# Performance work log

Measured on AMD Instinct MI355X. Metric: run time of the kernel, lower is better.

Reference implementation:

```python
import jax, jax.numpy as jnp
import numpy as np

U = 100000  # num_users
I = 100000  # num_items
D = 64      # dims
L = 50      # seq_L


def setup_inputs() -> dict:
    key = jax.random.key(0)
    ks = jax.random.split(key, 12)
    B, T = 4096, 100
    inp = {
        "user_ids": jax.random.randint(ks[0], (B,), 0, U),
        "item_seq_ids": jax.random.randint(ks[1], (B, L), 0, I),
        "target_item_ids": jax.random.randint(ks[2], (B, T), 0, I),
        # embedding tables (normal init)
        "user_table": jax.random.normal(ks[3], (U, D), jnp.float32) * 0.01,
        "item_table": jax.random.normal(ks[4], (I, D), jnp.float32) * 0.01,
        "W2_table": jax.random.normal(ks[5], (I, D), jnp.float32) * 0.01,
        "b2_table": jnp.zeros((I, 1), jnp.float32),
        # feature gates: Linear(dims, dims), he_uniform weight, zero bias
        "fg_item_W": jax.random.uniform(ks[6], (D, D), jnp.float32, -1.0, 1.0) * np.sqrt(6.0 / D),
        "fg_item_b": jnp.zeros((D,), jnp.float32),
        "fg_user_W": jax.random.uniform(ks[7], (D, D), jnp.float32, -1.0, 1.0) * np.sqrt(6.0 / D),
        "fg_user_b": jnp.zeros((D,), jnp.float32),
        # instance gates: xavier_uniform
        "inst_gate_item": jax.random.uniform(ks[8], (D, 1), jnp.float32, -1.0, 1.0) * np.sqrt(6.0 / (D + 1)),
        "inst_gate_user": jax.random.uniform(ks[9], (D, L), jnp.float32, -1.0, 1.0) * np.sqrt(6.0 / (D + L)),
    }
    return inp


def _forward_user(user_emb, item_embs, fg_item_W, fg_item_b, fg_user_W, fg_user_b,
                  inst_gate_item, inst_gate_user):
    # user_emb: [B,D], item_embs: [B,L,D]
    gate = jax.nn.sigmoid(
        item_embs @ fg_item_W.T + fg_item_b
        + (user_emb @ fg_user_W.T + fg_user_b)[:, None, :]
    )  # [B,L,D]
    gated = item_embs * gate  # [B,L,D]
    term1 = jnp.einsum("bld,d->bl", gated, inst_gate_item[:, 0])
    term2 = user_emb @ inst_gate_user  # [B,L]
    inst = jax.nn.sigmoid(term1 + term2)  # [B,L]
    union = jnp.sum(gated * inst[:, :, None], axis=1)  # [B,D]
    union = union / jnp.sum(inst, axis=1, keepdims=True)
    return union


def reference(user_ids, item_seq_ids, target_item_ids, user_table, item_table,
              W2_table, b2_table, fg_item_W, fg_item_b, fg_user_W, fg_user_b,
              inst_gate_item, inst_gate_user):
    item_embs = item_table[item_seq_ids]      # [B,L,D]
    user_emb = user_table[user_ids]           # [B,D]
    union = _forward_user(user_emb, item_embs, fg_item_W, fg_item_b,
                          fg_user_W, fg_user_b, inst_gate_item, inst_gate_user)
    w2 = W2_table[target_item_ids]            # [B,T,D]
    b2 = b2_table[target_item_ids][..., 0]    # [B,T]
    res = b2 + jnp.einsum("btd,bd->bt", w2, user_emb)
    res = res + jnp.einsum("bd,btd->bt", union, w2)
    # rel_score: bmm(item_embs, w2^T) summed over L == contract item_embs summed over L with w2
    res = res + jnp.einsum("bd,btd->bt", jnp.sum(item_embs, axis=1), w2)
    return res
```

## Files before the change

### kernel.cpp

```cpp
#include <hip/hip_runtime.h>

#define DD 64
#define LL 50
#define NB 4096
#define NT 100

typedef __attribute__((ext_vector_type(8))) __bf16 bf16x8;
typedef __attribute__((ext_vector_type(4))) float f32x4;

__device__ __forceinline__ float sigmoidf_(float x) {
    return __builtin_amdgcn_rcpf(1.0f + __expf(-x));
}
__device__ __forceinline__ unsigned pack_bf16(float hi, float lo) {
    union { float f; unsigned u; } a, b;
    a.f = hi; b.f = lo;
    return ((a.u + 0x8000u) & 0xffff0000u) | ((b.u + 0x8000u) >> 16);
}
__device__ __forceinline__ uint4 cvt8u(const float* f) {
    uint4 r;
    r.x = pack_bf16(f[1], f[0]);
    r.y = pack_bf16(f[3], f[2]);
    r.z = pack_bf16(f[5], f[4]);
    r.w = pack_bf16(f[7], f[6]);
    return r;
}
__device__ __forceinline__ bf16x8 cvt8(const float* f) {
    return __builtin_bit_cast(bf16x8, cvt8u(f));
}
__device__ __forceinline__ unsigned cvtpk(float lo, float hi) {
    unsigned r;
    asm("v_cvt_pk_bf16_f32 %0, %1, %2" : "=v"(r) : "v"(lo), "v"(hi));
    return r;
}
__device__ __forceinline__ bf16x8 cvt8f(const float* f) {
    uint4 r;
    r.x = cvtpk(f[0], f[1]);
    r.y = cvtpk(f[2], f[3]);
    r.z = cvtpk(f[4], f[5]);
    r.w = cvtpk(f[6], f[7]);
    return __builtin_bit_cast(bf16x8, r);
}
__device__ __forceinline__ void glds16(const float* g, float* l) {
    __builtin_amdgcn_global_load_lds(
        (const __attribute__((address_space(1))) void*)g,
        (__attribute__((address_space(3))) void*)l, 16, 0, 0);
}
__device__ __forceinline__ void glds4(const float* g, float* l) {
    __builtin_amdgcn_global_load_lds(
        (const __attribute__((address_space(1))) void*)g,
        (__attribute__((address_space(3))) void*)l, 4, 0, 0);
}

__global__ __launch_bounds__(128) void k0_user(
    const int* __restrict__ uid_g, const float* __restrict__ user_table,
    const float* __restrict__ Wu, const float* __restrict__ bu,
    const float* __restrict__ bi, const float* __restrict__ igu,
    const float* __restrict__ Wi,
    float* __restrict__ ufg_ws, float* __restrict__ t2_ws,
    unsigned short* __restrict__ wiB_ws)
{
    if (blockIdx.x == 256) {
        if (threadIdx.x >= 64) return;
        const int n = threadIdx.x;
        float tmp[64];
#pragma unroll
        for (int c4 = 0; c4 < 16; c4++)
            *(float4*)&tmp[c4 * 4] = *(const float4*)(Wi + n * DD + c4 * 4);
#pragma unroll
        for (int ch = 0; ch < 8; ch++)
            *(uint4*)(wiB_ws + n * DD + ch * 8) = cvt8u(tmp + ch * 8);
        return;
    }

    const int lane = threadIdx.x & 63;
    const int wv = threadIdx.x >> 6;
    const int c = lane & 15, q = lane >> 4;
    const int uid = uid_g[blockIdx.x * 16 + c];
    const float* urow = user_table + (size_t)uid * DD;

    bf16x8 af[2];
#pragma unroll
    for (int kf = 0; kf < 2; kf++) {
        float tmp[8];
        *(float4*)&tmp[0] = *(const float4*)(urow + kf * 32 + q * 8);
        *(float4*)&tmp[4] = *(const float4*)(urow + kf * 32 + q * 8 + 4);
        af[kf] = cvt8(tmp);
    }

#pragma unroll
    for (int ni0 = 0; ni0 < 4; ni0++) {
        const int ni = wv * 4 + ni0;
        f32x4 a = {0.f, 0.f, 0.f, 0.f};
#pragma unroll
        for (int kf = 0; kf < 2; kf++) {
            const int k0 = kf * 32 + q * 8;
            float tmp[8];
            if (ni < 4) {
                const float* src = Wu + (ni * 16 + c) * DD + k0;
                *(float4*)&tmp[0] = *(const float4*)src;
                *(float4*)&tmp[4] = *(const float4*)(src + 4);
            } else {
                const int l = ni * 16 + c - 64;
#pragma unroll
                for (int j = 0; j < 8; j++)
                    tmp[j] = (l < LL) ? igu[(k0 + j) * LL + l] : 0.f;
            }
            a = __builtin_amdgcn_mfma_f32_16x16x32_bf16(af[kf], cvt8(tmp), a, 0, 0, 0);
        }
        const int n = ni * 16 + c;
#pragma unroll
        for (int reg = 0; reg < 4; reg++) {
            const int bo = blockIdx.x * 16 + q * 4 + reg;
            if (n < DD)           ufg_ws[bo * DD + n] = a[reg] + bu[n] + bi[n];
            else if (n < DD + LL) t2_ws[bo * DD + (n - DD)] = a[reg];
        }
    }
}

__global__ __launch_bounds__(256, 4) void k1_fused(
    const int* __restrict__ uid_g, const int* __restrict__ iid_g,
    const int* __restrict__ tgt_g,
    const float* __restrict__ user_table, const float* __restrict__ item_table,
    const float* __restrict__ W2, const float* __restrict__ b2,
    const unsigned short* __restrict__ wiB, const float* __restrict__ igi,
    const float* __restrict__ ufg_ws, const float* __restrict__ t2_ws,
    float* __restrict__ out)
{
    const int tid = threadIdx.x;
    const int lane = tid & 63;
    const int w = tid >> 6;
    const int c = lane & 15, q = lane >> 4;
    const int j = tid & 15, gg = tid >> 4;
    const int b = blockIdx.x;

    __shared__ __align__(16) float sE[4][16 * DD];
    __shared__ __align__(16) float sB[128];
    __shared__ __align__(16) float sUu[DD];
    __shared__ __align__(16) float sU[4 * DD];
    __shared__ __align__(16) float sS[4 * DD];
    __shared__ float sI[4];
    __shared__ float sOut[112];

    const int* iidp = iid_g + b * LL;
    const int* tgtp = tgt_g + b * NT;
    float* sEw = sE[w];

    int iid4[4];
#pragma unroll
    for (int s = 0; s < 4; s++) {
        const int r = w * 16 + 4 * s + (lane >> 4);
        iid4[s] = iidp[r < LL ? r : LL - 1];
    }
    int tt[7];
#pragma unroll
    for (int i = 0; i < 7; i++) {
        const int ts = i * 16 + gg;
        tt[i] = tgtp[ts < NT ? ts : NT - 1];
    }

#pragma unroll
    for (int s = 0; s < 4; s++) {
        const int rl = 4 * s + (lane >> 4);
        const int j2 = (lane & 15) ^ (rl & 7);
        glds16(item_table + (size_t)iid4[s] * DD + j2 * 4, sEw + s * 256);
    }

    float4 wv[7];
#pragma unroll
    for (int i = 0; i < 7; i++)
        wv[i] = *(const float4*)(W2 + (size_t)tt[i] * DD + j * 4);

    if (w == 1) {
        const int uid = uid_g[b];
        glds4(user_table + (size_t)uid * DD + lane, sUu);
    }
    if (w == 2) {
        const int tb = lane < NT ? lane : NT - 1;
        glds4(b2 + tgtp[tb], sB);
    }
    if (w == 3) {
        const int sl = 64 + lane;
        const int tb = sl < NT ? sl : NT - 1;
        glds4(b2 + tgtp[tb], sB + 64);
    }

    float ufg4[4], igi4[4];
#pragma unroll
    for (int ni = 0; ni < 4; ni++) {
        ufg4[ni] = ufg_ws[b * DD + ni * 16 + c];
        igi4[ni] = igi[ni * 16 + c];
    }
    const float4 t2v = *(const float4*)(t2_ws + b * DD + w * 16 + q * 4);
    float t2a[4] = {t2v.x, t2v.y, t2v.z, t2v.w};

    bf16x8 wb[4][2];
#pragma unroll
    for (int ni = 0; ni < 4; ni++)
#pragma unroll
        for (int kf = 0; kf < 2; kf++)
            wb[ni][kf] = __builtin_bit_cast(bf16x8,
                *(const uint4*)(wiB + (ni * 16 + c) * DD + kf * 32 + q * 8));

    asm volatile("s_waitcnt vmcnt(0)" ::: "memory");
    __builtin_amdgcn_sched_barrier(0);

    bf16x8 ea[2];
    {
        const int grow = w * 16 + c;
        const float* rowp = sEw + c * DD;
        const int s7 = c & 7;
#pragma unroll
        for (int kf = 0; kf < 2; kf++) {
            float tmp[8];
            const int ch0 = (kf * 8 + 2 * q) ^ s7;
            const int ch1 = (kf * 8 + 2 * q + 1) ^ s7;
            *(float4*)&tmp[0] = *(const float4*)(rowp + ch0 * 4);
            *(float4*)&tmp[4] = *(const float4*)(rowp + ch1 * 4);
            if (grow >= LL) {
#pragma unroll
                for (int i = 0; i < 8; i++) tmp[i] = 0.f;
            }
            ea[kf] = cvt8f(tmp);
        }
    }

    float unum[4] = {0.f, 0.f, 0.f, 0.f};
    float sip[4]  = {0.f, 0.f, 0.f, 0.f};
    float isum = 0.f;
    {
        f32x4 acc[4];
#pragma unroll
        for (int ni = 0; ni < 4; ni++) {
            f32x4 a = {0.f, 0.f, 0.f, 0.f};
            a = __builtin_amdgcn_mfma_f32_16x16x32_bf16(ea[0], wb[ni][0], a, 0, 0, 0);
            a = __builtin_amdgcn_mfma_f32_16x16x32_bf16(ea[1], wb[ni][1], a, 0, 0, 0);
            acc[ni] = a;
        }
#pragma unroll
        for (int reg = 0; reg < 4; reg++) {
            const int lrl = q * 4 + reg;
            const int valid = (w * 16 + lrl < LL);
            const int s7 = lrl & 7;
            float gd[4];
            float t1 = 0.f;
#pragma unroll
            for (int ni = 0; ni < 4; ni++) {
                const int phys = (4 * ni + (c >> 2)) ^ s7;
                const float ev = sEw[lrl * DD + phys * 4 + (c & 3)];
                const float e = valid ? ev : 0.f;
                const float g = sigmoidf_(acc[ni][reg] + ufg4[ni]);
                gd[ni] = e * g;
                t1 += gd[ni] * igi4[ni];
                sip[ni] += e;
            }
            t1 += __shfl_xor(t1, 1); t1 += __shfl_xor(t1, 2);
            t1 += __shfl_xor(t1, 4); t1 += __shfl_xor(t1, 8);
            const float inst = valid ? sigmoidf_(t1 + t2a[reg]) : 0.f;
            isum += inst;
#pragma unroll
            for (int ni = 0; ni < 4; ni++)
                unum[ni] += gd[ni] * inst;
        }
    }

#pragma unroll
    for (int ni = 0; ni < 4; ni++) {
        unum[ni] += __shfl_xor(unum[ni], 16); unum[ni] += __shfl_xor(unum[ni], 32);
        sip[ni]  += __shfl_xor(sip[ni], 16);  sip[ni]  += __shfl_xor(sip[ni], 32);
    }
    isum += __shfl_xor(isum, 16); isum += __shfl_xor(isum, 32);

    const float un = (q == 0) ? unum[0] : (q == 1) ? unum[1] : (q == 2) ? unum[2] : unum[3];
    const float si = (q == 0) ? sip[0]  : (q == 1) ? sip[1]  : (q == 2) ? sip[2]  : sip[3];
    sU[w * DD + lane] = un;
    sS[w * DD + lane] = si;
    if (lane == 0) sI[w] = isum;
    __syncthreads();

    float4 vr;
    {
        const float4 u0 = *(const float4*)&sU[0 * DD + j * 4];
        const float4 u1 = *(const float4*)&sU[1 * DD + j * 4];
        const float4 u2 = *(const float4*)&sU[2 * DD + j * 4];
        const float4 u3 = *(const float4*)&sU[3 * DD + j * 4];
        const float4 s0 = *(const float4*)&sS[0 * DD + j * 4];
        const float4 s1 = *(const float4*)&sS[1 * DD + j * 4];
        const float4 s2 = *(const float4*)&sS[2 * DD + j * 4];
        const float4 s3 = *(const float4*)&sS[3 * DD + j * 4];
        const float4 uu = *(const float4*)&sUu[j * 4];
        const float rist = __builtin_amdgcn_rcpf(sI[0] + sI[1] + sI[2] + sI[3]);
        vr.x = uu.x + (u0.x + u1.x + u2.x + u3.x) * rist + (s0.x + s1.x + s2.x + s3.x);
        vr.y = uu.y + (u0.y + u1.y + u2.y + u3.y) * rist + (s0.y + s1.y + s2.y + s3.y);
        vr.z = uu.z + (u0.z + u1.z + u2.z + u3.z) * rist + (s0.z + s1.z + s2.z + s3.z);
        vr.w = uu.w + (u0.w + u1.w + u2.w + u3.w) * rist + (s0.w + s1.w + s2.w + s3.w);
    }

#pragma unroll
    for (int i = 0; i < 7; i++) {
        const int ts = i * 16 + gg;
        float s = wv[i].x * vr.x + wv[i].y * vr.y + wv[i].z * vr.z + wv[i].w * vr.w;
        s += __shfl_xor(s, 1); s += __shfl_xor(s, 2);
        s += __shfl_xor(s, 4); s += __shfl_xor(s, 8);
        if (j == 0 && ts < NT) sOut[ts] = s + sB[ts];
    }
    __syncthreads();
    if (tid < NT) out[b * NT + tid] = sOut[tid];
}

extern "C" void kernel_launch(void* const* d_in, const int* in_sizes, int n_in,
                              void* d_out, int out_size, void* d_ws, size_t ws_size,
                              hipStream_t stream)
{
    const int* user_ids        = (const int*)d_in[0];
    const int* item_seq_ids    = (const int*)d_in[1];
    const int* target_item_ids = (const int*)d_in[2];
    const float* user_tab      = (const float*)d_in[3];
    const float* item_tab      = (const float*)d_in[4];
    const float* W2_tab        = (const float*)d_in[5];
    const float* b2_tab        = (const float*)d_in[6];
    const float* fg_item_W     = (const float*)d_in[7];
    const float* fg_item_b     = (const float*)d_in[8];
    const float* fg_user_W     = (const float*)d_in[9];
    const float* fg_user_b     = (const float*)d_in[10];
    const float* igi           = (const float*)d_in[11];
    const float* igu           = (const float*)d_in[12];
    float* out = (float*)d_out;

    float* ufg_ws = (float*)d_ws;
    float* t2_ws  = ufg_ws + NB * DD;
    unsigned short* wiB_ws = (unsigned short*)(t2_ws + NB * DD);

    k0_user<<<257, 128, 0, stream>>>(user_ids, user_tab, fg_user_W, fg_user_b,
                                     fg_item_b, igu, fg_item_W,
                                     ufg_ws, t2_ws, wiB_ws);
    k1_fused<<<NB, 256, 0, stream>>>(user_ids, item_seq_ids, target_item_ids,
                                     user_tab, item_tab, W2_tab, b2_tab,
                                     wiB_ws, igi, ufg_ws, t2_ws, out);
}
```

Baseline: 153.6 us.

## Process four batch rows per block with double-buffered gather prefetch

k1_fused now handles NITER=4 batch rows per block, loading each next row's item embeddings, W2 rows, user row and biases into a second LDS/register buffer while the current row is computed. The fc_item weight copy and workspace values are pre-scaled by -log2(e), so each sigmoid uses exp2 directly instead of exp. The ufg workspace is stored in a permuted layout so each lane reads it with one float4 load. This trades a 4x smaller grid, doubled LDS and more registers (the occupancy hint of 4 blocks is dropped) for hiding gather latency and amortising the per-block weight loads.

```diff
diff --git a/kernel.cpp b/kernel.cpp
--- a/kernel.cpp
+++ b/kernel.cpp
@@ -4,12 +4,14 @@
 #define LL 50
 #define NB 4096
 #define NT 100
+#define NITER 4
+#define NEGK (-1.44269504088896f)
 
 typedef __attribute__((ext_vector_type(8))) __bf16 bf16x8;
 typedef __attribute__((ext_vector_type(4))) float f32x4;
 
-__device__ __forceinline__ float sigmoidf_(float x) {
-    return __builtin_amdgcn_rcpf(1.0f + __expf(-x));
+__device__ __forceinline__ float sig2_(float y) {
+    return __builtin_amdgcn_rcpf(1.0f + __builtin_amdgcn_exp2f(y));
 }
 __device__ __forceinline__ unsigned pack_bf16(float hi, float lo) {
     union { float f; unsigned u; } a, b;
@@ -67,6 +69,8 @@
         for (int c4 = 0; c4 < 16; c4++)
             *(float4*)&tmp[c4 * 4] = *(const float4*)(Wi + n * DD + c4 * 4);
 #pragma unroll
+        for (int kk = 0; kk < 64; kk++) tmp[kk] *= NEGK;
+#pragma unroll
         for (int ch = 0; ch < 8; ch++)
             *(uint4*)(wiB_ws + n * DD + ch * 8) = cvt8u(tmp + ch * 8);
         return;
@@ -102,8 +106,8 @@
             } else {
                 const int l = ni * 16 + c - 64;
 #pragma unroll
-                for (int j = 0; j < 8; j++)
-                    tmp[j] = (l < LL) ? igu[(k0 + j) * LL + l] : 0.f;
+                for (int jj = 0; jj < 8; jj++)
+                    tmp[jj] = (l < LL) ? igu[(k0 + jj) * LL + l] : 0.f;
             }
             a = __builtin_amdgcn_mfma_f32_16x16x32_bf16(af[kf], cvt8(tmp), a, 0, 0, 0);
         }
@@ -111,13 +115,15 @@
 #pragma unroll
         for (int reg = 0; reg < 4; reg++) {
             const int bo = blockIdx.x * 16 + q * 4 + reg;
-            if (n < DD)           ufg_ws[bo * DD + n] = a[reg] + bu[n] + bi[n];
-            else if (n < DD + LL) t2_ws[bo * DD + (n - DD)] = a[reg];
+            if (n < DD)
+                ufg_ws[bo * DD + (n & 15) * 4 + (n >> 4)] = NEGK * (a[reg] + bu[n] + bi[n]);
+            else if (n < DD + LL)
+                t2_ws[bo * DD + (n - DD)] = NEGK * a[reg];
         }
     }
 }
 
-__global__ __launch_bounds__(256, 4) void k1_fused(
+__global__ __launch_bounds__(256) void k1_fused(
     const int* __restrict__ uid_g, const int* __restrict__ iid_g,
     const int* __restrict__ tgt_g,
     const float* __restrict__ user_table, const float* __restrict__ item_table,
@@ -131,68 +137,19 @@
     const int w = tid >> 6;
     const int c = lane & 15, q = lane >> 4;
     const int j = tid & 15, gg = tid >> 4;
-    const int b = blockIdx.x;
-
-    __shared__ __align__(16) float sE[4][16 * DD];
-    __shared__ __align__(16) float sB[128];
-    __shared__ __align__(16) float sUu[DD];
+    const int b0 = blockIdx.x * NITER;
+
+    __shared__ __align__(16) float sE[2][4][16 * DD];
+    __shared__ __align__(16) float sUu[2][DD];
+    __shared__ __align__(16) float sB[2][128];
     __shared__ __align__(16) float sU[4 * DD];
     __shared__ __align__(16) float sS[4 * DD];
     __shared__ float sI[4];
     __shared__ float sOut[112];
 
-    const int* iidp = iid_g + b * LL;
-    const int* tgtp = tgt_g + b * NT;
-    float* sEw = sE[w];
-
-    int iid4[4];
-#pragma unroll
-    for (int s = 0; s < 4; s++) {
-        const int r = w * 16 + 4 * s + (lane >> 4);
-        iid4[s] = iidp[r < LL ? r : LL - 1];
-    }
-    int tt[7];
-#pragma unroll
-    for (int i = 0; i < 7; i++) {
-        const int ts = i * 16 + gg;
-        tt[i] = tgtp[ts < NT ? ts : NT - 1];
-    }
-
-#pragma unroll
-    for (int s = 0; s < 4; s++) {
-        const int rl = 4 * s + (lane >> 4);
-        const int j2 = (lane & 15) ^ (rl & 7);
-        glds16(item_table + (size_t)iid4[s] * DD + j2 * 4, sEw + s * 256);
-    }
-
-    float4 wv[7];
-#pragma unroll
-    for (int i = 0; i < 7; i++)
-        wv[i] = *(const float4*)(W2 + (size_t)tt[i] * DD + j * 4);
-
-    if (w == 1) {
-        const int uid = uid_g[b];
-        glds4(user_table + (size_t)uid * DD + lane, sUu);
-    }
-    if (w == 2) {
-        const int tb = lane < NT ? lane : NT - 1;
-        glds4(b2 + tgtp[tb], sB);
-    }
-    if (w == 3) {
-        const int sl = 64 + lane;
-        const int tb = sl < NT ? sl : NT - 1;
-        glds4(b2 + tgtp[tb], sB + 64);
-    }
-
-    float ufg4[4], igi4[4];
-#pragma unroll
-    for (int ni = 0; ni < 4; ni++) {
-        ufg4[ni] = ufg_ws[b * DD + ni * 16 + c];
-        igi4[ni] = igi[ni * 16 + c];
-    }
-    const float4 t2v = *(const float4*)(t2_ws + b * DD + w * 16 + q * 4);
-    float t2a[4] = {t2v.x, t2v.y, t2v.z, t2v.w};
-
+    float igi4[4];
+#pragma unroll
+    for (int ni = 0; ni < 4; ni++) igi4[ni] = igi[ni * 16 + c] * NEGK;
     bf16x8 wb[4][2];
 #pragma unroll
     for (int ni = 0; ni < 4; ni++)
@@ -201,110 +158,174 @@
             wb[ni][kf] = __builtin_bit_cast(bf16x8,
                 *(const uint4*)(wiB + (ni * 16 + c) * DD + kf * 32 + q * 8));
 
+    int iidA[4], ttA[7], uidA = 0, tqA = 0;
+    int iidB[4], ttB[7], uidB = 0, tqB = 0;
+    float4 wvb[2][7];
+    float4 ufgv[2], t2v[2];
+
+#define LOADQ(bb, iid_, tt_, uid_, tq_) do {                                   \
+        const int* iidp_ = iid_g + (bb) * LL;                                  \
+        const int* tgtp_ = tgt_g + (bb) * NT;                                  \
+        _Pragma("unroll") for (int s = 0; s < 4; s++) {                        \
+            const int r_ = w * 16 + 4 * s + q;                                 \
+            iid_[s] = iidp_[r_ < LL ? r_ : LL - 1]; }                          \
+        _Pragma("unroll") for (int i = 0; i < 7; i++) {                        \
+            const int ts_ = i * 16 + gg;                                       \
+            tt_[i] = tgtp_[ts_ < NT ? ts_ : NT - 1]; }                         \
+        uid_ = uid_g[bb];                                                      \
+        if (w == 2) tq_ = tgtp_[lane < NT ? lane : NT - 1];                    \
+        if (w == 3) { const int sl_ = 64 + lane;                               \
+                      tq_ = tgtp_[sl_ < NT ? sl_ : NT - 1]; }                  \
+    } while (0)
+
+#define ISSUEP(bb, p_, iid_, tt_, uid_, tq_) do {                              \
+        float* sEw_ = sE[p_][w];                                               \
+        _Pragma("unroll") for (int s = 0; s < 4; s++) {                        \
+            const int rl_ = 4 * s + q;                                         \
+            const int j2_ = c ^ (rl_ & 7);                                     \
+            glds16(item_table + (size_t)iid_[s] * DD + j2_ * 4,                \
+                   sEw_ + s * 256); }                                          \
+        _Pragma("unroll") for (int i = 0; i < 7; i++)                          \
+            wvb[p_][i] = *(const float4*)(W2 + (size_t)tt_[i] * DD + j * 4);   \
+        ufgv[p_] = *(const float4*)(ufg_ws + (size_t)(bb) * DD + c * 4);       \
+        t2v[p_]  = *(const float4*)(t2_ws + (size_t)(bb) * DD + w * 16 + q * 4);\
+        if (w == 1) glds4(user_table + (size_t)uid_ * DD + lane, sUu[p_]);     \
+        if (w == 2) glds4(b2 + tq_, sB[p_]);                                   \
+        if (w == 3) glds4(b2 + tq_, sB[p_] + 64);                              \
+    } while (0)
+
+    LOADQ(b0, iidA, ttA, uidA, tqA);
     asm volatile("s_waitcnt vmcnt(0)" ::: "memory");
     __builtin_amdgcn_sched_barrier(0);
-
-    bf16x8 ea[2];
-    {
-        const int grow = w * 16 + c;
-        const float* rowp = sEw + c * DD;
-        const int s7 = c & 7;
-#pragma unroll
-        for (int kf = 0; kf < 2; kf++) {
-            float tmp[8];
-            const int ch0 = (kf * 8 + 2 * q) ^ s7;
-            const int ch1 = (kf * 8 + 2 * q + 1) ^ s7;
-            *(float4*)&tmp[0] = *(const float4*)(rowp + ch0 * 4);
-            *(float4*)&tmp[4] = *(const float4*)(rowp + ch1 * 4);
-            if (grow >= LL) {
-#pragma unroll
-                for (int i = 0; i < 8; i++) tmp[i] = 0.f;
+    ISSUEP(b0, 0, iidA, ttA, uidA, tqA);
+    LOADQ(b0 + 1, iidB, ttB, uidB, tqB);
+
+#pragma unroll
+    for (int it = 0; it < NITER; ++it) {
+        const int p = it & 1;
+        const int bb = b0 + it;
+
+        asm volatile("s_waitcnt vmcnt(0)" ::: "memory");
+        __builtin_amdgcn_sched_barrier(0);
+
+        if (it + 1 < NITER) {
+            if ((it & 1) == 0) ISSUEP(bb + 1, 1, iidB, ttB, uidB, tqB);
+            else               ISSUEP(bb + 1, 0, iidA, ttA, uidA, tqA);
+        }
+        if (it + 2 < NITER) {
+            if ((it & 1) == 0) LOADQ(bb + 2, iidA, ttA, uidA, tqA);
+            else               LOADQ(bb + 2, iidB, ttB, uidB, tqB);
+        }
+
+        const float* sEw = sE[p][w];
+        const float ufg_n[4] = {ufgv[p].x, ufgv[p].y, ufgv[p].z, ufgv[p].w};
+        const float t2a[4]   = {t2v[p].x, t2v[p].y, t2v[p].z, t2v[p].w};
+
+        bf16x8 ea[2];
+        {
+            const int grow = w * 16 + c;
+            const float* rowp = sEw + c * DD;
+            const int s7 = c & 7;
+#pragma unroll
+            for (int kf = 0; kf < 2; kf++) {
+                float tmp[8];
+                const int ch0 = (kf * 8 + 2 * q) ^ s7;
+                const int ch1 = (kf * 8 + 2 * q + 1) ^ s7;
+                *(float4*)&tmp[0] = *(const float4*)(rowp + ch0 * 4);
+                *(float4*)&tmp[4] = *(const float4*)(rowp + ch1 * 4);
+                if (grow >= LL) {
+#pragma unroll
+                    for (int i = 0; i < 8; i++) tmp[i] = 0.f;
+                }
+                ea[kf] = cvt8f(tmp);
             }
-            ea[kf] = cvt8f(tmp);
-        }
+        }
+
+        float unum[4] = {0.f, 0.f, 0.f, 0.f};
+        float sip[4]  = {0.f, 0.f, 0.f, 0.f};
+        float isum = 0.f;
+        {
+            f32x4 acc[4];
+#pragma unroll
+            for (int ni = 0; ni < 4; ni++) {
+                f32x4 a = {0.f, 0.f, 0.f, 0.f};
+                a = __builtin_amdgcn_mfma_f32_16x16x32_bf16(ea[0], wb[ni][0], a, 0, 0, 0);
+                a = __builtin_amdgcn_mfma_f32_16x16x32_bf16(ea[1], wb[ni][1], a, 0, 0, 0);
+                acc[ni] = a;
+            }
+#pragma unroll
+            for (int reg = 0; reg < 4; reg++) {
+                const int lrl = q * 4 + reg;
+                const int valid = (w * 16 + lrl < LL);
+                const int s7 = lrl & 7;
+                float gd[4];
+                float t1 = 0.f;
+#pragma unroll
+                for (int ni = 0; ni < 4; ni++) {
+                    const int phys = (4 * ni + (c >> 2)) ^ s7;
+                    const float ev = sEw[lrl * DD + phys * 4 + (c & 3)];
+                    const float e = valid ? ev : 0.f;
+                    const float g = sig2_(acc[ni][reg] + ufg_n[ni]);
+                    gd[ni] = e * g;
+                    t1 += gd[ni] * igi4[ni];
+                    sip[ni] += e;
+                }
+                t1 += __shfl_xor(t1, 1); t1 += __shfl_xor(t1, 2);
+                t1 += __shfl_xor(t1, 4); t1 += __shfl_xor(t1, 8);
+                const float inst = valid ? sig2_(t1 + t2a[reg]) : 0.f;
+                isum += inst;
+#pragma unroll
+                for (int ni = 0; ni < 4; ni++)
+                    unum[ni] += gd[ni] * inst;
+            }
+        }
+
+#pragma unroll
+        for (int ni = 0; ni < 4; ni++) {
+            unum[ni] += __shfl_xor(unum[ni], 16); unum[ni] += __shfl_xor(unum[ni], 32);
+            sip[ni]  += __shfl_xor(sip[ni], 16);  sip[ni]  += __shfl_xor(sip[ni], 32);
+        }
+        isum += __shfl_xor(isum, 16); isum += __shfl_xor(isum, 32);
+
+        const float un = (q == 0) ? unum[0] : (q == 1) ? unum[1] : (q == 2) ? unum[2] : unum[3];
+        const float si = (q == 0) ? sip[0]  : (q == 1) ? sip[1]  : (q == 2) ? sip[2]  : sip[3];
+        sU[w * DD + lane] = un;
+        sS[w * DD + lane] = si;
+        if (lane == 0) sI[w] = isum;
+        __syncthreads();
+
+        float4 vr;
+        {
+            const float4 u0 = *(const float4*)&sU[0 * DD + j * 4];
+            const float4 u1 = *(const float4*)&sU[1 * DD + j * 4];
+            const float4 u2 = *(const float4*)&sU[2 * DD + j * 4];
+            const float4 u3 = *(const float4*)&sU[3 * DD + j * 4];
+            const float4 s0 = *(const float4*)&sS[0 * DD + j * 4];
+            const float4 s1 = *(const float4*)&sS[1 * DD + j * 4];
+            const float4 s2 = *(const float4*)&sS[2 * DD + j * 4];
+            const float4 s3 = *(const float4*)&sS[3 * DD + j * 4];
+            const float4 uu = *(const float4*)&sUu[p][j * 4];
+            const float rist = __builtin_amdgcn_rcpf(sI[0] + sI[1] + sI[2] + sI[3]);
+            vr.x = uu.x + (u0.x + u1.x + u2.x + u3.x) * rist + (s0.x + s1.x + s2.x + s3.x);
+            vr.y = uu.y + (u0.y + u1.y + u2.y + u3.y) * rist + (s0.y + s1.y + s2.y + s3.y);
+            vr.z = uu.z + (u0.z + u1.z + u2.z + u3.z) * rist + (s0.z + s1.z + s2.z + s3.z);
+            vr.w = uu.w + (u0.w + u1.w + u2.w + u3.w) * rist + (s0.w + s1.w + s2.w + s3.w);
+        }
+
+#pragma unroll
+        for (int i = 0; i < 7; i++) {
+            const int ts = i * 16 + gg;
+            float s = wvb[p][i].x * vr.x + wvb[p][i].y * vr.y
+                    + wvb[p][i].z * vr.z + wvb[p][i].w * vr.w;
+            s += __shfl_xor(s, 1); s += __shfl_xor(s, 2);
+            s += __shfl_xor(s, 4); s += __shfl_xor(s, 8);
+            if (j == 0 && ts < NT) sOut[ts] = s + sB[p][ts];
+        }
+        __syncthreads();
+        if (tid < NT) out[bb * NT + tid] = sOut[tid];
     }
-
-    float unum[4] = {0.f, 0.f, 0.f, 0.f};
-    float sip[4]  = {0.f, 0.f, 0.f, 0.f};
-    float isum = 0.f;
-    {
-        f32x4 acc[4];
-#pragma unroll
-        for (int ni = 0; ni < 4; ni++) {
-            f32x4 a = {0.f, 0.f, 0.f, 0.f};
-            a = __builtin_amdgcn_mfma_f32_16x16x32_bf16(ea[0], wb[ni][0], a, 0, 0, 0);
-            a = __builtin_amdgcn_mfma_f32_16x16x32_bf16(ea[1], wb[ni][1], a, 0, 0, 0);
-            acc[ni] = a;
-        }
-#pragma unroll
-        for (int reg = 0; reg < 4; reg++) {
-            const int lrl = q * 4 + reg;
-            const int valid = (w * 16 + lrl < LL);
-            const int s7 = lrl & 7;
-            float gd[4];
-            float t1 = 0.f;
-#pragma unroll
-            for (int ni = 0; ni < 4; ni++) {
-                const int phys = (4 * ni + (c >> 2)) ^ s7;
-                const float ev = sEw[lrl * DD + phys * 4 + (c & 3)];
-                const float e = valid ? ev : 0.f;
-                const float g = sigmoidf_(acc[ni][reg] + ufg4[ni]);
-                gd[ni] = e * g;
-                t1 += gd[ni] * igi4[ni];
-                sip[ni] += e;
-            }
-            t1 += __shfl_xor(t1, 1); t1 += __shfl_xor(t1, 2);
-            t1 += __shfl_xor(t1, 4); t1 += __shfl_xor(t1, 8);
-            const float inst = valid ? sigmoidf_(t1 + t2a[reg]) : 0.f;
-            isum += inst;
-#pragma unroll
-            for (int ni = 0; ni < 4; ni++)
-                unum[ni] += gd[ni] * inst;
-        }
-    }
-
-#pragma unroll
-    for (int ni = 0; ni < 4; ni++) {
-        unum[ni] += __shfl_xor(unum[ni], 16); unum[ni] += __shfl_xor(unum[ni], 32);
-        sip[ni]  += __shfl_xor(sip[ni], 16);  sip[ni]  += __shfl_xor(sip[ni], 32);
-    }
-    isum += __shfl_xor(isum, 16); isum += __shfl_xor(isum, 32);
-
-    const float un = (q == 0) ? unum[0] : (q == 1) ? unum[1] : (q == 2) ? unum[2] : unum[3];
-    const float si = (q == 0) ? sip[0]  : (q == 1) ? sip[1]  : (q == 2) ? sip[2]  : sip[3];
-    sU[w * DD + lane] = un;
-    sS[w * DD + lane] = si;
-    if (lane == 0) sI[w] = isum;
-    __syncthreads();
-
-    float4 vr;
-    {
-        const float4 u0 = *(const float4*)&sU[0 * DD + j * 4];
-        const float4 u1 = *(const float4*)&sU[1 * DD + j * 4];
-        const float4 u2 = *(const float4*)&sU[2 * DD + j * 4];
-        const float4 u3 = *(const float4*)&sU[3 * DD + j * 4];
-        const float4 s0 = *(const float4*)&sS[0 * DD + j * 4];
-        const float4 s1 = *(const float4*)&sS[1 * DD + j * 4];
-        const float4 s2 = *(const float4*)&sS[2 * DD + j * 4];
-        const float4 s3 = *(const float4*)&sS[3 * DD + j * 4];
-        const float4 uu = *(const float4*)&sUu[j * 4];
-        const float rist = __builtin_amdgcn_rcpf(sI[0] + sI[1] + sI[2] + sI[3]);
-        vr.x = uu.x + (u0.x + u1.x + u2.x + u3.x) * rist + (s0.x + s1.x + s2.x + s3.x);
-        vr.y = uu.y + (u0.y + u1.y + u2.y + u3.y) * rist + (s0.y + s1.y + s2.y + s3.y);
-        vr.z = uu.z + (u0.z + u1.z + u2.z + u3.z) * rist + (s0.z + s1.z + s2.z + s3.z);
-        vr.w = uu.w + (u0.w + u1.w + u2.w + u3.w) * rist + (s0.w + s1.w + s2.w + s3.w);
-    }
-
-#pragma unroll
-    for (int i = 0; i < 7; i++) {
-        const int ts = i * 16 + gg;
-        float s = wv[i].x * vr.x + wv[i].y * vr.y + wv[i].z * vr.z + wv[i].w * vr.w;
-        s += __shfl_xor(s, 1); s += __shfl_xor(s, 2);
-        s += __shfl_xor(s, 4); s += __shfl_xor(s, 8);
-        if (j == 0 && ts < NT) sOut[ts] = s + sB[ts];
-    }
-    __syncthreads();
-    if (tid < NT) out[b * NT + tid] = sOut[tid];
+#undef LOADQ
+#undef ISSUEP
 }
 
 extern "C" void kernel_launch(void* const* d_in, const int* in_sizes, int n_in,
@@ -333,7 +354,7 @@
     k0_user<<<257, 128, 0, stream>>>(user_ids, user_tab, fg_user_W, fg_user_b,
                                      fg_item_b, igu, fg_item_W,
                                      ufg_ws, t2_ws, wiB_ws);
-    k1_fused<<<NB, 256, 0, stream>>>(user_ids, item_seq_ids, target_item_ids,
-                                     user_tab, item_tab, W2_tab, b2_tab,
-                                     wiB_ws, igi, ufg_ws, t2_ws, out);
-}
+    k1_fused<<<NB / NITER, 256, 0, stream>>>(user_ids, item_seq_ids, target_item_ids,
+                                             user_tab, item_tab, W2_tab, b2_tab,
+                                             wiB_ws, igi, ufg_ws, t2_ws, out);
+}
```

After: 160.2 us. 4.3% more time.

## Fuse user-projection prekernel into main kernel, computing gate terms per block

Applied to the files above, without the earlier changes.

Removes the separate k0_user launch and its workspace round trip. Each block of the main kernel now computes the user feature-gate projection and the instance-gate user term in fp32 with shuffle reductions, shares them through LDS behind a barrier, and converts the item gate weights to bf16 in-block. This saves a kernel launch and the dependency between the two kernels. In exchange it repeats the weight loads and conversion in every block, adds a __syncthreads, and drops the explicit vmcnt wait.

```diff
diff --git a/kernel.cpp b/kernel.cpp
--- a/kernel.cpp
+++ b/kernel.cpp
@@ -10,22 +10,6 @@
 
 __device__ __forceinline__ float sigmoidf_(float x) {
     return __builtin_amdgcn_rcpf(1.0f + __expf(-x));
-}
-__device__ __forceinline__ unsigned pack_bf16(float hi, float lo) {
-    union { float f; unsigned u; } a, b;
-    a.f = hi; b.f = lo;
-    return ((a.u + 0x8000u) & 0xffff0000u) | ((b.u + 0x8000u) >> 16);
-}
-__device__ __forceinline__ uint4 cvt8u(const float* f) {
-    uint4 r;
-    r.x = pack_bf16(f[1], f[0]);
-    r.y = pack_bf16(f[3], f[2]);
-    r.z = pack_bf16(f[5], f[4]);
-    r.w = pack_bf16(f[7], f[6]);
-    return r;
-}
-__device__ __forceinline__ bf16x8 cvt8(const float* f) {
-    return __builtin_bit_cast(bf16x8, cvt8u(f));
 }
 __device__ __forceinline__ unsigned cvtpk(float lo, float hi) {
     unsigned r;
@@ -51,79 +35,14 @@
         (__attribute__((address_space(3))) void*)l, 4, 0, 0);
 }
 
-__global__ __launch_bounds__(128) void k0_user(
-    const int* __restrict__ uid_g, const float* __restrict__ user_table,
-    const float* __restrict__ Wu, const float* __restrict__ bu,
-    const float* __restrict__ bi, const float* __restrict__ igu,
-    const float* __restrict__ Wi,
-    float* __restrict__ ufg_ws, float* __restrict__ t2_ws,
-    unsigned short* __restrict__ wiB_ws)
-{
-    if (blockIdx.x == 256) {
-        if (threadIdx.x >= 64) return;
-        const int n = threadIdx.x;
-        float tmp[64];
-#pragma unroll
-        for (int c4 = 0; c4 < 16; c4++)
-            *(float4*)&tmp[c4 * 4] = *(const float4*)(Wi + n * DD + c4 * 4);
-#pragma unroll
-        for (int ch = 0; ch < 8; ch++)
-            *(uint4*)(wiB_ws + n * DD + ch * 8) = cvt8u(tmp + ch * 8);
-        return;
-    }
-
-    const int lane = threadIdx.x & 63;
-    const int wv = threadIdx.x >> 6;
-    const int c = lane & 15, q = lane >> 4;
-    const int uid = uid_g[blockIdx.x * 16 + c];
-    const float* urow = user_table + (size_t)uid * DD;
-
-    bf16x8 af[2];
-#pragma unroll
-    for (int kf = 0; kf < 2; kf++) {
-        float tmp[8];
-        *(float4*)&tmp[0] = *(const float4*)(urow + kf * 32 + q * 8);
-        *(float4*)&tmp[4] = *(const float4*)(urow + kf * 32 + q * 8 + 4);
-        af[kf] = cvt8(tmp);
-    }
-
-#pragma unroll
-    for (int ni0 = 0; ni0 < 4; ni0++) {
-        const int ni = wv * 4 + ni0;
-        f32x4 a = {0.f, 0.f, 0.f, 0.f};
-#pragma unroll
-        for (int kf = 0; kf < 2; kf++) {
-            const int k0 = kf * 32 + q * 8;
-            float tmp[8];
-            if (ni < 4) {
-                const float* src = Wu + (ni * 16 + c) * DD + k0;
-                *(float4*)&tmp[0] = *(const float4*)src;
-                *(float4*)&tmp[4] = *(const float4*)(src + 4);
-            } else {
-                const int l = ni * 16 + c - 64;
-#pragma unroll
-                for (int j = 0; j < 8; j++)
-                    tmp[j] = (l < LL) ? igu[(k0 + j) * LL + l] : 0.f;
-            }
-            a = __builtin_amdgcn_mfma_f32_16x16x32_bf16(af[kf], cvt8(tmp), a, 0, 0, 0);
-        }
-        const int n = ni * 16 + c;
-#pragma unroll
-        for (int reg = 0; reg < 4; reg++) {
-            const int bo = blockIdx.x * 16 + q * 4 + reg;
-            if (n < DD)           ufg_ws[bo * DD + n] = a[reg] + bu[n] + bi[n];
-            else if (n < DD + LL) t2_ws[bo * DD + (n - DD)] = a[reg];
-        }
-    }
-}
-
-__global__ __launch_bounds__(256, 4) void k1_fused(
+__global__ __launch_bounds__(256, 4) void k_all(
     const int* __restrict__ uid_g, const int* __restrict__ iid_g,
     const int* __restrict__ tgt_g,
     const float* __restrict__ user_table, const float* __restrict__ item_table,
     const float* __restrict__ W2, const float* __restrict__ b2,
-    const unsigned short* __restrict__ wiB, const float* __restrict__ igi,
-    const float* __restrict__ ufg_ws, const float* __restrict__ t2_ws,
+    const float* __restrict__ Wu, const float* __restrict__ bu,
+    const float* __restrict__ bi, const float* __restrict__ igu,
+    const float* __restrict__ Wi, const float* __restrict__ igi,
     float* __restrict__ out)
 {
     const int tid = threadIdx.x;
@@ -136,6 +55,7 @@
     __shared__ __align__(16) float sE[4][16 * DD];
     __shared__ __align__(16) float sB[128];
     __shared__ __align__(16) float sUu[DD];
+    __shared__ __align__(16) float sUFG[DD];
     __shared__ __align__(16) float sU[4 * DD];
     __shared__ __align__(16) float sS[4 * DD];
     __shared__ float sI[4];
@@ -144,11 +64,12 @@
     const int* iidp = iid_g + b * LL;
     const int* tgtp = tgt_g + b * NT;
     float* sEw = sE[w];
+    const int uid = uid_g[b];
 
     int iid4[4];
 #pragma unroll
     for (int s = 0; s < 4; s++) {
-        const int r = w * 16 + 4 * s + (lane >> 4);
+        const int r = w * 16 + 4 * s + q;
         iid4[s] = iidp[r < LL ? r : LL - 1];
     }
     int tt[7];
@@ -160,8 +81,8 @@
 
 #pragma unroll
     for (int s = 0; s < 4; s++) {
-        const int rl = 4 * s + (lane >> 4);
-        const int j2 = (lane & 15) ^ (rl & 7);
+        const int rl = 4 * s + q;
+        const int j2 = c ^ (rl & 7);
         glds16(item_table + (size_t)iid4[s] * DD + j2 * 4, sEw + s * 256);
     }
 
@@ -170,10 +91,8 @@
     for (int i = 0; i < 7; i++)
         wv[i] = *(const float4*)(W2 + (size_t)tt[i] * DD + j * 4);
 
-    if (w == 1) {
-        const int uid = uid_g[b];
+    if (w == 1)
         glds4(user_table + (size_t)uid * DD + lane, sUu);
-    }
     if (w == 2) {
         const int tb = lane < NT ? lane : NT - 1;
         glds4(b2 + tgtp[tb], sB);
@@ -184,25 +103,51 @@
         glds4(b2 + tgtp[tb], sB + 64);
     }
 
-    float ufg4[4], igi4[4];
-#pragma unroll
-    for (int ni = 0; ni < 4; ni++) {
-        ufg4[ni] = ufg_ws[b * DD + ni * 16 + c];
-        igi4[ni] = igi[ni * 16 + c];
-    }
-    const float4 t2v = *(const float4*)(t2_ws + b * DD + w * 16 + q * 4);
-    float t2a[4] = {t2v.x, t2v.y, t2v.z, t2v.w};
+    const int nl = lane >> 2, kq = lane & 3, k0i = kq * 16;
+    const int nglob = w * 16 + nl;
+    const int ltc = nglob < LL ? nglob : LL - 1;
+    const float* urow = user_table + (size_t)uid * DD;
+
+    float u16[16], wu16[16];
+#pragma unroll
+    for (int m = 0; m < 4; m++)
+        *(float4*)&u16[m * 4] = *(const float4*)(urow + k0i + m * 4);
+#pragma unroll
+    for (int m = 0; m < 4; m++)
+        *(float4*)&wu16[m * 4] = *(const float4*)(Wu + nglob * DD + k0i + m * 4);
+
+    float ufg_p = 0.f, t2_p = 0.f;
+#pragma unroll
+    for (int m = 0; m < 16; m++) {
+        ufg_p += u16[m] * wu16[m];
+        t2_p  += u16[m] * igu[(k0i + m) * LL + ltc];
+    }
+    ufg_p += __shfl_xor(ufg_p, 1); ufg_p += __shfl_xor(ufg_p, 2);
+    t2_p  += __shfl_xor(t2_p, 1);  t2_p  += __shfl_xor(t2_p, 2);
+    const float t2full = t2_p;
+    if ((lane & 3) == 0)
+        sUFG[nglob] = ufg_p + bu[nglob] + bi[nglob];
 
     bf16x8 wb[4][2];
 #pragma unroll
     for (int ni = 0; ni < 4; ni++)
 #pragma unroll
-        for (int kf = 0; kf < 2; kf++)
-            wb[ni][kf] = __builtin_bit_cast(bf16x8,
-                *(const uint4*)(wiB + (ni * 16 + c) * DD + kf * 32 + q * 8));
-
-    asm volatile("s_waitcnt vmcnt(0)" ::: "memory");
-    __builtin_amdgcn_sched_barrier(0);
+        for (int kf = 0; kf < 2; kf++) {
+            float tmp[8];
+            const float* src = Wi + (ni * 16 + c) * DD + kf * 32 + q * 8;
+            *(float4*)&tmp[0] = *(const float4*)src;
+            *(float4*)&tmp[4] = *(const float4*)(src + 4);
+            wb[ni][kf] = cvt8f(tmp);
+        }
+    float igi4[4];
+#pragma unroll
+    for (int ni = 0; ni < 4; ni++) igi4[ni] = igi[ni * 16 + c];
+
+    __syncthreads();
+
+    float ufg4[4];
+#pragma unroll
+    for (int ni = 0; ni < 4; ni++) ufg4[ni] = sUFG[ni * 16 + c];
 
     bf16x8 ea[2];
     {
@@ -255,7 +200,8 @@
             }
             t1 += __shfl_xor(t1, 1); t1 += __shfl_xor(t1, 2);
             t1 += __shfl_xor(t1, 4); t1 += __shfl_xor(t1, 8);
-            const float inst = valid ? sigmoidf_(t1 + t2a[reg]) : 0.f;
+            const float t2a = __shfl(t2full, (q * 4 + reg) << 2);
+            const float inst = valid ? sigmoidf_(t1 + t2a) : 0.f;
             isum += inst;
 #pragma unroll
             for (int ni = 0; ni < 4; ni++)
@@ -326,14 +272,8 @@
     const float* igu           = (const float*)d_in[12];
     float* out = (float*)d_out;
 
-    float* ufg_ws = (float*)d_ws;
-    float* t2_ws  = ufg_ws + NB * DD;
-    unsigned short* wiB_ws = (unsigned short*)(t2_ws + NB * DD);
-
-    k0_user<<<257, 128, 0, stream>>>(user_ids, user_tab, fg_user_W, fg_user_b,
-                                     fg_item_b, igu, fg_item_W,
-                                     ufg_ws, t2_ws, wiB_ws);
-    k1_fused<<<NB, 256, 0, stream>>>(user_ids, item_seq_ids, target_item_ids,
-                                     user_tab, item_tab, W2_tab, b2_tab,
-                                     wiB_ws, igi, ufg_ws, t2_ws, out);
-}
+    k_all<<<NB, 256, 0, stream>>>(user_ids, item_seq_ids, target_item_ids,
+                                  user_tab, item_tab, W2_tab, b2_tab,
+                                  fg_user_W, fg_user_b, fg_item_b, igu,
+                                  fg_item_W, igi, out);
+}
```

New measurement: 171.4 us. 11.6% more time.

## Fuse per-user gate projection into main kernel, shrink prologue to weight packing

Applied to the files above, without the earlier changes.

Replaces the 257-block user projection kernel with a single-block pack kernel. That kernel converts fg_user_W and the transposed inst_gate_user to bf16 and precomputes the combined bias. The main kernel now gathers the user row itself and computes the user feature-gate and term2 projections with MFMAs. The per-row results are redistributed with shuffles. This removes the ufg/t2 workspace round-trip through global memory and most of the first kernel's work. In exchange, each block does redundant MFMAs, each wave loads more weight fragments, and register pressure rises.

```diff
diff --git a/kernel.cpp b/kernel.cpp
--- a/kernel.cpp
+++ b/kernel.cpp
@@ -24,9 +24,6 @@
     r.w = pack_bf16(f[7], f[6]);
     return r;
 }
-__device__ __forceinline__ bf16x8 cvt8(const float* f) {
-    return __builtin_bit_cast(bf16x8, cvt8u(f));
-}
 __device__ __forceinline__ unsigned cvtpk(float lo, float hi) {
     unsigned r;
     asm("v_cvt_pk_bf16_f32 %0, %1, %2" : "=v"(r) : "v"(lo), "v"(hi));
@@ -40,80 +37,64 @@
     r.w = cvtpk(f[6], f[7]);
     return __builtin_bit_cast(bf16x8, r);
 }
-__device__ __forceinline__ void glds16(const float* g, float* l) {
+__device__ __forceinline__ void glds16(const void* g, void* l) {
     __builtin_amdgcn_global_load_lds(
         (const __attribute__((address_space(1))) void*)g,
         (__attribute__((address_space(3))) void*)l, 16, 0, 0);
 }
-__device__ __forceinline__ void glds4(const float* g, float* l) {
+__device__ __forceinline__ void glds4(const void* g, void* l) {
     __builtin_amdgcn_global_load_lds(
         (const __attribute__((address_space(1))) void*)g,
         (__attribute__((address_space(3))) void*)l, 4, 0, 0);
 }
 
-__global__ __launch_bounds__(128) void k0_user(
-    const int* __restrict__ uid_g, const float* __restrict__ user_table,
-    const float* __restrict__ Wu, const float* __restrict__ bu,
-    const float* __restrict__ bi, const float* __restrict__ igu,
-    const float* __restrict__ Wi,
-    float* __restrict__ ufg_ws, float* __restrict__ t2_ws,
-    unsigned short* __restrict__ wiB_ws)
+__global__ __launch_bounds__(256) void k_pack(
+    const float* __restrict__ Wi, const float* __restrict__ Wu,
+    const float* __restrict__ bu, const float* __restrict__ bi,
+    const float* __restrict__ igu,
+    unsigned short* __restrict__ wiB, unsigned short* __restrict__ wuB,
+    float* __restrict__ biasArr)
 {
-    if (blockIdx.x == 256) {
-        if (threadIdx.x >= 64) return;
-        const int n = threadIdx.x;
+    __shared__ float sT[64][52];
+    const int tid = threadIdx.x;
+    const int g = tid >> 6, n = tid & 63;
+
+    if (g == 0) {
         float tmp[64];
 #pragma unroll
         for (int c4 = 0; c4 < 16; c4++)
             *(float4*)&tmp[c4 * 4] = *(const float4*)(Wi + n * DD + c4 * 4);
 #pragma unroll
         for (int ch = 0; ch < 8; ch++)
-            *(uint4*)(wiB_ws + n * DD + ch * 8) = cvt8u(tmp + ch * 8);
-        return;
-    }
-
-    const int lane = threadIdx.x & 63;
-    const int wv = threadIdx.x >> 6;
-    const int c = lane & 15, q = lane >> 4;
-    const int uid = uid_g[blockIdx.x * 16 + c];
-    const float* urow = user_table + (size_t)uid * DD;
-
-    bf16x8 af[2];
-#pragma unroll
-    for (int kf = 0; kf < 2; kf++) {
-        float tmp[8];
-        *(float4*)&tmp[0] = *(const float4*)(urow + kf * 32 + q * 8);
-        *(float4*)&tmp[4] = *(const float4*)(urow + kf * 32 + q * 8 + 4);
-        af[kf] = cvt8(tmp);
-    }
-
-#pragma unroll
-    for (int ni0 = 0; ni0 < 4; ni0++) {
-        const int ni = wv * 4 + ni0;
-        f32x4 a = {0.f, 0.f, 0.f, 0.f};
-#pragma unroll
-        for (int kf = 0; kf < 2; kf++) {
-            const int k0 = kf * 32 + q * 8;
-            float tmp[8];
-            if (ni < 4) {
-                const float* src = Wu + (ni * 16 + c) * DD + k0;
-                *(float4*)&tmp[0] = *(const float4*)src;
-                *(float4*)&tmp[4] = *(const float4*)(src + 4);
-            } else {
-                const int l = ni * 16 + c - 64;
-#pragma unroll
-                for (int j = 0; j < 8; j++)
-                    tmp[j] = (l < LL) ? igu[(k0 + j) * LL + l] : 0.f;
-            }
-            a = __builtin_amdgcn_mfma_f32_16x16x32_bf16(af[kf], cvt8(tmp), a, 0, 0, 0);
-        }
-        const int n = ni * 16 + c;
-#pragma unroll
-        for (int reg = 0; reg < 4; reg++) {
-            const int bo = blockIdx.x * 16 + q * 4 + reg;
-            if (n < DD)           ufg_ws[bo * DD + n] = a[reg] + bu[n] + bi[n];
-            else if (n < DD + LL) t2_ws[bo * DD + (n - DD)] = a[reg];
-        }
+            *(uint4*)(wiB + n * DD + ch * 8) = cvt8u(tmp + ch * 8);
+    } else if (g == 1) {
+        float tmp[64];
+#pragma unroll
+        for (int c4 = 0; c4 < 16; c4++)
+            *(float4*)&tmp[c4 * 4] = *(const float4*)(Wu + n * DD + c4 * 4);
+#pragma unroll
+        for (int ch = 0; ch < 8; ch++)
+            *(uint4*)(wuB + n * DD + ch * 8) = cvt8u(tmp + ch * 8);
+    } else if (g == 2) {
+#pragma unroll
+        for (int l = 0; l < LL; l++) sT[n][l] = igu[n * LL + l];
+    } else {
+        biasArr[n] = bu[n] + bi[n];
+    }
+    __syncthreads();
+    if (g == 2 && n < LL) {
+        float tmp[64];
+#pragma unroll
+        for (int k = 0; k < 64; k++) tmp[k] = sT[k][n];
+#pragma unroll
+        for (int ch = 0; ch < 8; ch++)
+            *(uint4*)(wuB + (64 + n) * DD + ch * 8) = cvt8u(tmp + ch * 8);
+    }
+    if (g == 3 && n < 14) {
+        const uint4 z = {0u, 0u, 0u, 0u};
+#pragma unroll
+        for (int ch = 0; ch < 8; ch++)
+            *(uint4*)(wuB + (114 + n) * DD + ch * 8) = z;
     }
 }
 
@@ -122,8 +103,8 @@
     const int* __restrict__ tgt_g,
     const float* __restrict__ user_table, const float* __restrict__ item_table,
     const float* __restrict__ W2, const float* __restrict__ b2,
-    const unsigned short* __restrict__ wiB, const float* __restrict__ igi,
-    const float* __restrict__ ufg_ws, const float* __restrict__ t2_ws,
+    const unsigned short* __restrict__ wiB, const unsigned short* __restrict__ wuB,
+    const float* __restrict__ biasArr, const float* __restrict__ igi,
     float* __restrict__ out)
 {
     const int tid = threadIdx.x;
@@ -144,11 +125,12 @@
     const int* iidp = iid_g + b * LL;
     const int* tgtp = tgt_g + b * NT;
     float* sEw = sE[w];
+    const int uid = uid_g[b];
 
     int iid4[4];
 #pragma unroll
     for (int s = 0; s < 4; s++) {
-        const int r = w * 16 + 4 * s + (lane >> 4);
+        const int r = w * 16 + 4 * s + q;
         iid4[s] = iidp[r < LL ? r : LL - 1];
     }
     int tt[7];
@@ -160,8 +142,8 @@
 
 #pragma unroll
     for (int s = 0; s < 4; s++) {
-        const int rl = 4 * s + (lane >> 4);
-        const int j2 = (lane & 15) ^ (rl & 7);
+        const int rl = 4 * s + q;
+        const int j2 = c ^ (rl & 7);
         glds16(item_table + (size_t)iid4[s] * DD + j2 * 4, sEw + s * 256);
     }
 
@@ -170,10 +152,8 @@
     for (int i = 0; i < 7; i++)
         wv[i] = *(const float4*)(W2 + (size_t)tt[i] * DD + j * 4);
 
-    if (w == 1) {
-        const int uid = uid_g[b];
+    if (w == 1)
         glds4(user_table + (size_t)uid * DD + lane, sUu);
-    }
     if (w == 2) {
         const int tb = lane < NT ? lane : NT - 1;
         glds4(b2 + tgtp[tb], sB);
@@ -184,14 +164,31 @@
         glds4(b2 + tgtp[tb], sB + 64);
     }
 
-    float ufg4[4], igi4[4];
-#pragma unroll
-    for (int ni = 0; ni < 4; ni++) {
-        ufg4[ni] = ufg_ws[b * DD + ni * 16 + c];
-        igi4[ni] = igi[ni * 16 + c];
-    }
-    const float4 t2v = *(const float4*)(t2_ws + b * DD + w * 16 + q * 4);
-    float t2a[4] = {t2v.x, t2v.y, t2v.z, t2v.w};
+    const float* urow = user_table + (size_t)uid * DD;
+    bf16x8 af[2];
+#pragma unroll
+    for (int kf = 0; kf < 2; kf++) {
+        float tmp[8];
+        *(float4*)&tmp[0] = *(const float4*)(urow + kf * 32 + q * 8);
+        *(float4*)&tmp[4] = *(const float4*)(urow + kf * 32 + q * 8 + 4);
+        af[kf] = cvt8f(tmp);
+    }
+    bf16x8 wg5[5][2];
+#pragma unroll
+    for (int ng = 0; ng < 5; ng++) {
+        const int row = (ng < 4) ? (ng * 16 + c) : (64 + w * 16 + c);
+#pragma unroll
+        for (int kf = 0; kf < 2; kf++)
+            wg5[ng][kf] = __builtin_bit_cast(bf16x8,
+                *(const uint4*)(wuB + row * DD + kf * 32 + q * 8));
+    }
+    float biasv[4];
+#pragma unroll
+    for (int ni = 0; ni < 4; ni++) biasv[ni] = biasArr[ni * 16 + c];
+
+    float igi4[4];
+#pragma unroll
+    for (int ni = 0; ni < 4; ni++) igi4[ni] = igi[ni * 16 + c];
 
     bf16x8 wb[4][2];
 #pragma unroll
@@ -203,6 +200,24 @@
 
     asm volatile("s_waitcnt vmcnt(0)" ::: "memory");
     __builtin_amdgcn_sched_barrier(0);
+
+    float ufg4[4], t2val;
+    {
+        f32x4 fa[5];
+#pragma unroll
+        for (int ng = 0; ng < 5; ng++) {
+            f32x4 a = {0.f, 0.f, 0.f, 0.f};
+            a = __builtin_amdgcn_mfma_f32_16x16x32_bf16(af[0], wg5[ng][0], a, 0, 0, 0);
+            a = __builtin_amdgcn_mfma_f32_16x16x32_bf16(af[1], wg5[ng][1], a, 0, 0, 0);
+            fa[ng] = a;
+        }
+#pragma unroll
+        for (int ni = 0; ni < 4; ni++) ufg4[ni] = fa[ni][0] + biasv[ni];
+        t2val = fa[4][0];
+    }
+    float t2a[4];
+#pragma unroll
+    for (int reg = 0; reg < 4; reg++) t2a[reg] = __shfl(t2val, q * 4 + reg);
 
     bf16x8 ea[2];
     {
@@ -326,14 +341,13 @@
     const float* igu           = (const float*)d_in[12];
     float* out = (float*)d_out;
 
-    float* ufg_ws = (float*)d_ws;
-    float* t2_ws  = ufg_ws + NB * DD;
-    unsigned short* wiB_ws = (unsigned short*)(t2_ws + NB * DD);
-
-    k0_user<<<257, 128, 0, stream>>>(user_ids, user_tab, fg_user_W, fg_user_b,
-                                     fg_item_b, igu, fg_item_W,
-                                     ufg_ws, t2_ws, wiB_ws);
+    unsigned short* wiB_ws  = (unsigned short*)d_ws;
+    unsigned short* wuB_ws  = wiB_ws + 64 * 64;
+    float* bias_ws          = (float*)(wuB_ws + 128 * 64);
+
+    k_pack<<<1, 256, 0, stream>>>(fg_item_W, fg_user_W, fg_user_b, fg_item_b,
+                                  igu, wiB_ws, wuB_ws, bias_ws);
     k1_fused<<<NB, 256, 0, stream>>>(user_ids, item_seq_ids, target_item_ids,
                                      user_tab, item_tab, W2_tab, b2_tab,
-                                     wiB_ws, igi, ufg_ws, t2_ws, out);
-}
+                                     wiB_ws, wuB_ws, bias_ws, igi, out);
+}
```

After: 166.6 us. 1.08x slower.
